# Kernel tuning notes

Measured on AMD Instinct MI355X. Metric: run time of the kernel, lower is better.

## Reference

```python
import jax, jax.numpy as jnp
import numpy as np

B, T, FC, FX = 64, 1024, 256, 512

def setup_inputs() -> dict:
    key = jax.random.key(0)
    kC, kX, kW, kb = jax.random.split(key, 4)
    C = jax.random.normal(kC, (B, T, FC), dtype=jnp.float32)
    X = jax.random.normal(kX, (B, T, FX), dtype=jnp.float32)
    # nn.Linear(encoding_size, context_size): W [fc, fx], b [fc]
    lim = 1.0 / np.sqrt(FX)
    W = jax.random.uniform(kW, (FC, FX), minval=-lim, maxval=lim, dtype=jnp.float32)
    b = jax.random.uniform(kb, (FC,), minval=-lim, maxval=lim, dtype=jnp.float32)
    return {"C": C, "X": X, "W": W, "b": b}

def reference(C, X, W, b):
    # Xt = Linear(X): [B, T, fc]
    Xt = jnp.einsum('btx,cx->btc', X, W) + b
    # Z[i, j, t] = <C[i, t, :], Xt[j, t, :]>  -> per-timestep BxB similarity
    Z = jnp.einsum('itc,jtc->ijt', C, Xt)
    # logsumexp over the negatives axis (dim 1), numerically stable
    lse = jax.nn.logsumexp(Z, axis=1)          # [B, T]
    Zdiag = jnp.einsum('iit->it', Z)           # [B, T], Z[i, i, t]
    return jnp.mean(Zdiag - lse)
```

## Files before the change

kernel.cpp:

```cpp
#include <hip/hip_runtime.h>

#define B_  64
#define T_  1024
#define FC_ 256
#define FX_ 512

typedef __bf16 bf16x8 __attribute__((ext_vector_type(8)));
typedef float  f32x4  __attribute__((ext_vector_type(4)));

__device__ __forceinline__ unsigned short f2bf(float f) {
  union { float f; unsigned int u; } v; v.f = f;
  unsigned int r = v.u + 0x7fffu + ((v.u >> 16) & 1u);
  return (unsigned short)(r >> 16);
}
__device__ __forceinline__ unsigned int pk2(float lo, float hi) {
  return (unsigned int)f2bf(lo) | ((unsigned int)f2bf(hi) << 16);
}

__global__ void k_wcvt(const float* __restrict__ W, unsigned short* __restrict__ Wb) {
  const int i = blockIdx.x * 256 + threadIdx.x;
  float4 v = ((const float4*)W)[i];
  ushort4 h;
  h.x = f2bf(v.x); h.y = f2bf(v.y); h.z = f2bf(v.z); h.w = f2bf(v.w);
  ((ushort4*)Wb)[i] = h;
}

__global__ __launch_bounds__(512, 2)
void k_fused(const float* __restrict__ C, const float* __restrict__ X,
             const unsigned short* __restrict__ Wb, const float* __restrict__ bias,
             float* __restrict__ out)
{
  __shared__ __align__(16) char sMem[81920];
  char* sX0 = sMem;
  char* sX1 = sMem + 8192;
  char* sW0 = sMem + 16384;
  char* sW1 = sMem + 49152;
  char* sC  = sMem;
  char* sXt = sMem + 32768;

  const int t    = blockIdx.x;
  const int tid  = threadIdx.x;
  const int lane = tid & 63;
  const int wid  = tid >> 6;

  const int xrow  = tid >> 3;
  const int xcol  = (tid & 7) * 8;
  const float* xbase = X + ((size_t)xrow * T_ + t) * FX_ + xcol;
  float4 x0a = *(const float4*)(xbase);
  float4 x0b = *(const float4*)(xbase + 4);

  const int wsw = (((lane & 7) ^ (lane >> 3)) << 4);
  {
    const char* wb0 = (const char*)Wb;
    #pragma unroll
    for (int l = 0; l < 4; ++l) {
      const int seg = wid * 4 + l;
      const int c   = seg * 8 + (lane >> 3);
      __builtin_amdgcn_global_load_lds(
          (const __attribute__((address_space(1))) unsigned int*)(wb0 + c * 1024 + wsw),
          (__attribute__((address_space(3))) unsigned int*)(sW0 + seg * 1024),
          16, 0, 0);
    }
  }

  const int crow = tid >> 3;
  const int ccol = (tid & 7) * 32;
  const float* cbase = C + ((size_t)crow * T_ + t) * FC_ + ccol;
  float4 creg[8];
  #pragma unroll
  for (int q = 0; q < 8; ++q) creg[q] = *(const float4*)(cbase + 4 * q);

  const float bv0 = bias[wid * 32 + (lane & 15)];
  const float bv1 = bias[wid * 32 + 16 + (lane & 15)];

  asm volatile("" ::: "memory");

  const int xwoff = xrow * 128 + (((tid & 7) * 16) ^ ((xrow & 7) << 4));
  {
    uint4 pk;
    pk.x = pk2(x0a.x, x0a.y); pk.y = pk2(x0a.z, x0a.w);
    pk.z = pk2(x0b.x, x0b.y); pk.w = pk2(x0b.z, x0b.w);
    *(uint4*)(sX0 + xwoff) = pk;
  }
  __syncthreads();

  f32x4 acc[4][2];
  #pragma unroll
  for (int i = 0; i < 4; ++i)
    #pragma unroll
    for (int n2 = 0; n2 < 2; ++n2)
      #pragma unroll
      for (int r = 0; r < 4; ++r) acc[i][n2][r] = 0.f;

  #pragma unroll 2
  for (int k = 0; k < 8; ++k) {
    char* scx = (k & 1) ? sX1 : sX0;
    char* snx = (k & 1) ? sX0 : sX1;
    char* scw = (k & 1) ? sW1 : sW0;
    char* snw = (k & 1) ? sW0 : sW1;

    float4 xn0, xn1;
    if (k < 7) {
      xn0 = *(const float4*)(xbase + (k + 1) * 64);
      xn1 = *(const float4*)(xbase + (k + 1) * 64 + 4);
      const char* wbk = (const char*)Wb + (k + 1) * 128;
      #pragma unroll
      for (int l = 0; l < 4; ++l) {
        const int seg = wid * 4 + l;
        const int c   = seg * 8 + (lane >> 3);
        __builtin_amdgcn_global_load_lds(
            (const __attribute__((address_space(1))) unsigned int*)(wbk + c * 1024 + wsw),
            (__attribute__((address_space(3))) unsigned int*)(snw + seg * 1024),
            16, 0, 0);
      }
    }
    asm volatile("" ::: "memory");

    #pragma unroll
    for (int kk = 0; kk < 2; ++kk) {
      const int kb = kk * 64 + ((lane >> 4) << 4);
      bf16x8 a[4], b2[2];
      #pragma unroll
      for (int i = 0; i < 4; ++i) {
        const int ar = i * 16 + (lane & 15);
        a[i] = *(const bf16x8*)(scx + ar * 128 + (kb ^ ((ar & 7) << 4)));
      }
      #pragma unroll
      for (int n2 = 0; n2 < 2; ++n2) {
        const int br = wid * 32 + n2 * 16 + (lane & 15);
        b2[n2] = *(const bf16x8*)(scw + br * 128 + (kb ^ ((br & 7) << 4)));
      }
      #pragma unroll
      for (int i = 0; i < 4; ++i)
        #pragma unroll
        for (int n2 = 0; n2 < 2; ++n2)
          acc[i][n2] = __builtin_amdgcn_mfma_f32_16x16x32_bf16(a[i], b2[n2], acc[i][n2], 0, 0, 0);
    }

    if (k < 7) {
      uint4 pk;
      pk.x = pk2(xn0.x, xn0.y); pk.y = pk2(xn0.z, xn0.w);
      pk.z = pk2(xn1.x, xn1.y); pk.w = pk2(xn1.z, xn1.w);
      *(uint4*)(snx + xwoff) = pk;
    }
    __syncthreads();
  }

  #pragma unroll
  for (int i = 0; i < 4; ++i)
    #pragma unroll
    for (int n2 = 0; n2 < 2; ++n2) {
      const int c  = wid * 32 + n2 * 16 + (lane & 15);
      const float bb = (n2 == 0) ? bv0 : bv1;
      #pragma unroll
      for (int r = 0; r < 4; ++r) {
        const int j   = i * 16 + ((lane >> 4) << 2) + r;
        const int off = j * 512 + ((2 * c) ^ ((j & 7) << 4));
        *(unsigned short*)(sXt + off) = f2bf(acc[i][n2][r] + bb);
      }
    }
  #pragma unroll
  for (int q = 0; q < 4; ++q) {
    const int cb  = (tid & 7) * 64 + q * 16;
    const int off = crow * 512 + (cb ^ ((crow & 7) << 4));
    float4 a0 = creg[2 * q], a1 = creg[2 * q + 1];
    uint4 pk;
    pk.x = pk2(a0.x, a0.y); pk.y = pk2(a0.z, a0.w);
    pk.z = pk2(a1.x, a1.y); pk.w = pk2(a1.z, a1.w);
    *(uint4*)(sC + off) = pk;
  }
  __syncthreads();

  if (wid < 4) {
    f32x4 z[4];
    #pragma unroll
    for (int n = 0; n < 4; ++n)
      #pragma unroll
      for (int r = 0; r < 4; ++r) z[n][r] = 0.f;

    #pragma unroll
    for (int kk = 0; kk < 8; ++kk) {
      const int kb = kk * 64 + ((lane >> 4) << 4);
      const int ar = wid * 16 + (lane & 15);
      bf16x8 a = *(const bf16x8*)(sC + ar * 512 + (kb ^ ((ar & 7) << 4)));
      #pragma unroll
      for (int n = 0; n < 4; ++n) {
        const int br = n * 16 + (lane & 15);
        bf16x8 b = *(const bf16x8*)(sXt + br * 512 + (kb ^ ((br & 7) << 4)));
        z[n] = __builtin_amdgcn_mfma_f32_16x16x32_bf16(a, b, z[n], 0, 0, 0);
      }
    }

    float partial = 0.f;
    #pragma unroll
    for (int r = 0; r < 4; ++r) {
      float m = fmaxf(fmaxf(z[0][r], z[1][r]), fmaxf(z[2][r], z[3][r]));
      #pragma unroll
      for (int d = 1; d < 16; d <<= 1) m = fmaxf(m, __shfl_xor(m, d));
      float s = __expf(z[0][r] - m) + __expf(z[1][r] - m) +
                __expf(z[2][r] - m) + __expf(z[3][r] - m);
      #pragma unroll
      for (int d = 1; d < 16; d <<= 1) s += __shfl_xor(s, d);
      const float lse = m + __logf(s);
      float dv = 0.f;
      #pragma unroll
      for (int n = 0; n < 4; ++n) dv = (n == wid) ? z[n][r] : dv;
      const int dl = ((lane >> 4) << 2) + r;
      if ((lane & 15) == dl) partial += dv - lse;
    }
    #pragma unroll
    for (int d = 1; d < 64; d <<= 1) partial += __shfl_xor(partial, d);
    if (lane == 0) atomicAdd(out, partial * (1.0f / (B_ * T_)));
  }
}

extern "C" void kernel_launch(void* const* d_in, const int* in_sizes, int n_in,
                              void* d_out, int out_size, void* d_ws, size_t ws_size,
                              hipStream_t stream) {
  const float* C  = (const float*)d_in[0];
  const float* X  = (const float*)d_in[1];
  const float* W  = (const float*)d_in[2];
  const float* bb = (const float*)d_in[3];
  unsigned short* Wb = (unsigned short*)d_ws;
  float* out = (float*)d_out;

  hipMemsetAsync(out, 0, sizeof(float), stream);
  k_wcvt <<<dim3(128),  dim3(256), 0, stream>>>(W, Wb);
  k_fused<<<dim3(1024), dim3(512), 0, stream>>>(C, X, Wb, bb, out);
}
```

Before: 271.5 us.

## Shrink fused block to 256 threads, read W fragments directly from global

The fused kernel moves from 512 threads to 256 threads per block and from 80KB to 40KB of LDS, targeting four blocks per CU instead of two. W fragments are now loaded straight from global/L2 into registers rather than staged through LDS with global_load_lds. X is single-buffered with register prefetch, and C is loaded into registers and fed directly as MFMA A operands instead of going through LDS. The memset launch is folded into the weight-conversion kernel. This raises occupancy and cuts LDS traffic, at the cost of uncoalesced per-lane global W reads and more syncs per k step.

```diff
diff --git a/kernel.cpp b/kernel.cpp
--- a/kernel.cpp
+++ b/kernel.cpp
@@ -16,202 +16,189 @@
 __device__ __forceinline__ unsigned int pk2(float lo, float hi) {
   return (unsigned int)f2bf(lo) | ((unsigned int)f2bf(hi) << 16);
 }
-
-__global__ void k_wcvt(const float* __restrict__ W, unsigned short* __restrict__ Wb) {
+__device__ __forceinline__ uint4 pk8(float4 a, float4 b) {
+  uint4 p;
+  p.x = pk2(a.x, a.y); p.y = pk2(a.z, a.w);
+  p.z = pk2(b.x, b.y); p.w = pk2(b.z, b.w);
+  return p;
+}
+
+__global__ void k_wcvt(const float* __restrict__ W, unsigned short* __restrict__ Wb,
+                       float* __restrict__ out) {
   const int i = blockIdx.x * 256 + threadIdx.x;
   float4 v = ((const float4*)W)[i];
   ushort4 h;
   h.x = f2bf(v.x); h.y = f2bf(v.y); h.z = f2bf(v.z); h.w = f2bf(v.w);
   ((ushort4*)Wb)[i] = h;
-}
-
-__global__ __launch_bounds__(512, 2)
+  if (i == 0) out[0] = 0.f;
+}
+
+__global__ __launch_bounds__(256, 4)
 void k_fused(const float* __restrict__ C, const float* __restrict__ X,
              const unsigned short* __restrict__ Wb, const float* __restrict__ bias,
              float* __restrict__ out)
 {
-  __shared__ __align__(16) char sMem[81920];
-  char* sX0 = sMem;
-  char* sX1 = sMem + 8192;
-  char* sW0 = sMem + 16384;
-  char* sW1 = sMem + 49152;
-  char* sC  = sMem;
-  char* sXt = sMem + 32768;
+  __shared__ __align__(16) char sMem[40960];
+  char* sX  = sMem;
+  char* sXt = sMem + 8192;
 
   const int t    = blockIdx.x;
   const int tid  = threadIdx.x;
   const int lane = tid & 63;
   const int wid  = tid >> 6;
-
-  const int xrow  = tid >> 3;
-  const int xcol  = (tid & 7) * 8;
-  const float* xbase = X + ((size_t)xrow * T_ + t) * FX_ + xcol;
-  float4 x0a = *(const float4*)(xbase);
-  float4 x0b = *(const float4*)(xbase + 4);
-
-  const int wsw = (((lane & 7) ^ (lane >> 3)) << 4);
+  const int l15  = lane & 15;
+  const int lhi  = lane >> 4;
+
+  const int xrow = tid >> 2;
+  const int xcb  = (tid & 3) * 32;
+  const float* xptr = X + ((size_t)xrow * T_ + t) * FX_ + ((tid & 3) << 4);
+  const int xwbase = xrow * 128;
+  const int xsw    = (xrow & 7) << 4;
+
+  const char* wbase = (const char*)Wb + (size_t)(wid * 64 + l15) * 1024 + lhi * 16;
+
+  float bv[4];
+  #pragma unroll
+  for (int n2 = 0; n2 < 4; ++n2) bv[n2] = bias[wid * 64 + n2 * 16 + l15];
+
+  float4 xb[4];
   {
-    const char* wb0 = (const char*)Wb;
-    #pragma unroll
-    for (int l = 0; l < 4; ++l) {
-      const int seg = wid * 4 + l;
-      const int c   = seg * 8 + (lane >> 3);
-      __builtin_amdgcn_global_load_lds(
-          (const __attribute__((address_space(1))) unsigned int*)(wb0 + c * 1024 + wsw),
-          (__attribute__((address_space(3))) unsigned int*)(sW0 + seg * 1024),
-          16, 0, 0);
-    }
-  }
-
-  const int crow = tid >> 3;
-  const int ccol = (tid & 7) * 32;
-  const float* cbase = C + ((size_t)crow * T_ + t) * FC_ + ccol;
-  float4 creg[8];
-  #pragma unroll
-  for (int q = 0; q < 8; ++q) creg[q] = *(const float4*)(cbase + 4 * q);
-
-  const float bv0 = bias[wid * 32 + (lane & 15)];
-  const float bv1 = bias[wid * 32 + 16 + (lane & 15)];
-
-  asm volatile("" ::: "memory");
-
-  const int xwoff = xrow * 128 + (((tid & 7) * 16) ^ ((xrow & 7) << 4));
-  {
-    uint4 pk;
-    pk.x = pk2(x0a.x, x0a.y); pk.y = pk2(x0a.z, x0a.w);
-    pk.z = pk2(x0b.x, x0b.y); pk.w = pk2(x0b.z, x0b.w);
-    *(uint4*)(sX0 + xwoff) = pk;
-  }
+    float4 xa[4];
+    #pragma unroll
+    for (int q = 0; q < 4; ++q) xa[q] = *(const float4*)(xptr + q * 4);
+    #pragma unroll
+    for (int q = 0; q < 4; ++q) xb[q] = *(const float4*)(xptr + 64 + q * 4);
+    uint4 p0 = pk8(xa[0], xa[1]);
+    uint4 p1 = pk8(xa[2], xa[3]);
+    *(uint4*)(sX + xwbase + ((xcb +  0) ^ xsw)) = p0;
+    *(uint4*)(sX + xwbase + ((xcb + 16) ^ xsw)) = p1;
+  }
+
+  f32x4 acc[4][4];
+  #pragma unroll
+  for (int i = 0; i < 4; ++i)
+    #pragma unroll
+    for (int n2 = 0; n2 < 4; ++n2)
+      #pragma unroll
+      for (int r = 0; r < 4; ++r) acc[i][n2][r] = 0.f;
+
   __syncthreads();
 
-  f32x4 acc[4][2];
+  #pragma unroll
+  for (int k = 0; k < 8; ++k) {
+    #pragma unroll
+    for (int kk = 0; kk < 2; ++kk) {
+      bf16x8 afr[4];
+      #pragma unroll
+      for (int i = 0; i < 4; ++i) {
+        const int ar = i * 16 + l15;
+        afr[i] = *(const bf16x8*)(sX + ar * 128 + ((kk * 64 + lhi * 16) ^ ((ar & 7) << 4)));
+      }
+      #pragma unroll
+      for (int n2 = 0; n2 < 4; ++n2) {
+        bf16x8 w = *(const bf16x8*)(wbase + n2 * 16384 + k * 128 + kk * 64);
+        #pragma unroll
+        for (int i = 0; i < 4; ++i)
+          acc[i][n2] = __builtin_amdgcn_mfma_f32_16x16x32_bf16(afr[i], w, acc[i][n2], 0, 0, 0);
+      }
+    }
+    __syncthreads();
+    if (k < 7) {
+      float4 xn[4];
+      if (k < 6) {
+        #pragma unroll
+        for (int q = 0; q < 4; ++q) xn[q] = *(const float4*)(xptr + (k + 2) * 64 + q * 4);
+      }
+      uint4 p0 = pk8(xb[0], xb[1]);
+      uint4 p1 = pk8(xb[2], xb[3]);
+      *(uint4*)(sX + xwbase + ((xcb +  0) ^ xsw)) = p0;
+      *(uint4*)(sX + xwbase + ((xcb + 16) ^ xsw)) = p1;
+      __syncthreads();
+      if (k < 6) {
+        #pragma unroll
+        for (int q = 0; q < 4; ++q) xb[q] = xn[q];
+      }
+    }
+  }
+
+  const float* cptr = C + ((size_t)(wid * 16 + l15) * T_ + t) * FC_ + lhi * 8;
+  float4 cv[8];
+  #pragma unroll
+  for (int q = 0; q < 4; ++q) {
+    cv[2 * q]     = *(const float4*)(cptr + q * 32);
+    cv[2 * q + 1] = *(const float4*)(cptr + q * 32 + 4);
+  }
+
   #pragma unroll
   for (int i = 0; i < 4; ++i)
     #pragma unroll
-    for (int n2 = 0; n2 < 2; ++n2)
-      #pragma unroll
-      for (int r = 0; r < 4; ++r) acc[i][n2][r] = 0.f;
-
-  #pragma unroll 2
-  for (int k = 0; k < 8; ++k) {
-    char* scx = (k & 1) ? sX1 : sX0;
-    char* snx = (k & 1) ? sX0 : sX1;
-    char* scw = (k & 1) ? sW1 : sW0;
-    char* snw = (k & 1) ? sW0 : sW1;
-
-    float4 xn0, xn1;
-    if (k < 7) {
-      xn0 = *(const float4*)(xbase + (k + 1) * 64);
-      xn1 = *(const float4*)(xbase + (k + 1) * 64 + 4);
-      const char* wbk = (const char*)Wb + (k + 1) * 128;
-      #pragma unroll
-      for (int l = 0; l < 4; ++l) {
-        const int seg = wid * 4 + l;
-        const int c   = seg * 8 + (lane >> 3);
-        __builtin_amdgcn_global_load_lds(
-            (const __attribute__((address_space(1))) unsigned int*)(wbk + c * 1024 + wsw),
-            (__attribute__((address_space(3))) unsigned int*)(snw + seg * 1024),
-            16, 0, 0);
-      }
-    }
-    asm volatile("" ::: "memory");
-
-    #pragma unroll
-    for (int kk = 0; kk < 2; ++kk) {
-      const int kb = kk * 64 + ((lane >> 4) << 4);
-      bf16x8 a[4], b2[2];
-      #pragma unroll
-      for (int i = 0; i < 4; ++i) {
-        const int ar = i * 16 + (lane & 15);
-        a[i] = *(const bf16x8*)(scx + ar * 128 + (kb ^ ((ar & 7) << 4)));
-      }
-      #pragma unroll
-      for (int n2 = 0; n2 < 2; ++n2) {
-        const int br = wid * 32 + n2 * 16 + (lane & 15);
-        b2[n2] = *(const bf16x8*)(scw + br * 128 + (kb ^ ((br & 7) << 4)));
-      }
-      #pragma unroll
-      for (int i = 0; i < 4; ++i)
-        #pragma unroll
-        for (int n2 = 0; n2 < 2; ++n2)
-          acc[i][n2] = __builtin_amdgcn_mfma_f32_16x16x32_bf16(a[i], b2[n2], acc[i][n2], 0, 0, 0);
-    }
-
-    if (k < 7) {
-      uint4 pk;
-      pk.x = pk2(xn0.x, xn0.y); pk.y = pk2(xn0.z, xn0.w);
-      pk.z = pk2(xn1.x, xn1.y); pk.w = pk2(xn1.z, xn1.w);
-      *(uint4*)(snx + xwoff) = pk;
-    }
-    __syncthreads();
-  }
-
-  #pragma unroll
-  for (int i = 0; i < 4; ++i)
-    #pragma unroll
-    for (int n2 = 0; n2 < 2; ++n2) {
-      const int c  = wid * 32 + n2 * 16 + (lane & 15);
-      const float bb = (n2 == 0) ? bv0 : bv1;
+    for (int n2 = 0; n2 < 4; ++n2) {
+      const int c2 = (wid * 64 + n2 * 16 + l15) * 2;
       #pragma unroll
       for (int r = 0; r < 4; ++r) {
-        const int j   = i * 16 + ((lane >> 4) << 2) + r;
-        const int off = j * 512 + ((2 * c) ^ ((j & 7) << 4));
-        *(unsigned short*)(sXt + off) = f2bf(acc[i][n2][r] + bb);
-      }
-    }
-  #pragma unroll
-  for (int q = 0; q < 4; ++q) {
-    const int cb  = (tid & 7) * 64 + q * 16;
-    const int off = crow * 512 + (cb ^ ((crow & 7) << 4));
-    float4 a0 = creg[2 * q], a1 = creg[2 * q + 1];
-    uint4 pk;
-    pk.x = pk2(a0.x, a0.y); pk.y = pk2(a0.z, a0.w);
-    pk.z = pk2(a1.x, a1.y); pk.w = pk2(a1.z, a1.w);
-    *(uint4*)(sC + off) = pk;
+        const int j = i * 16 + lhi * 4 + r;
+        *(unsigned short*)(sXt + j * 512 + (c2 ^ ((j & 7) << 4))) =
+            f2bf(acc[i][n2][r] + bv[n2]);
+      }
+    }
+
+  bf16x8 ca[4];
+  #pragma unroll
+  for (int q = 0; q < 4; ++q) ca[q] = __builtin_bit_cast(bf16x8, pk8(cv[2 * q], cv[2 * q + 1]));
+  float4 cw[8];
+  #pragma unroll
+  for (int q = 0; q < 4; ++q) {
+    cw[2 * q]     = *(const float4*)(cptr + 128 + q * 32);
+    cw[2 * q + 1] = *(const float4*)(cptr + 128 + q * 32 + 4);
   }
   __syncthreads();
 
-  if (wid < 4) {
-    f32x4 z[4];
-    #pragma unroll
-    for (int n = 0; n < 4; ++n)
-      #pragma unroll
-      for (int r = 0; r < 4; ++r) z[n][r] = 0.f;
-
-    #pragma unroll
-    for (int kk = 0; kk < 8; ++kk) {
-      const int kb = kk * 64 + ((lane >> 4) << 4);
-      const int ar = wid * 16 + (lane & 15);
-      bf16x8 a = *(const bf16x8*)(sC + ar * 512 + (kb ^ ((ar & 7) << 4)));
-      #pragma unroll
-      for (int n = 0; n < 4; ++n) {
-        const int br = n * 16 + (lane & 15);
-        bf16x8 b = *(const bf16x8*)(sXt + br * 512 + (kb ^ ((br & 7) << 4)));
-        z[n] = __builtin_amdgcn_mfma_f32_16x16x32_bf16(a, b, z[n], 0, 0, 0);
-      }
-    }
-
-    float partial = 0.f;
-    #pragma unroll
-    for (int r = 0; r < 4; ++r) {
-      float m = fmaxf(fmaxf(z[0][r], z[1][r]), fmaxf(z[2][r], z[3][r]));
-      #pragma unroll
-      for (int d = 1; d < 16; d <<= 1) m = fmaxf(m, __shfl_xor(m, d));
-      float s = __expf(z[0][r] - m) + __expf(z[1][r] - m) +
-                __expf(z[2][r] - m) + __expf(z[3][r] - m);
-      #pragma unroll
-      for (int d = 1; d < 16; d <<= 1) s += __shfl_xor(s, d);
-      const float lse = m + __logf(s);
-      float dv = 0.f;
-      #pragma unroll
-      for (int n = 0; n < 4; ++n) dv = (n == wid) ? z[n][r] : dv;
-      const int dl = ((lane >> 4) << 2) + r;
-      if ((lane & 15) == dl) partial += dv - lse;
-    }
-    #pragma unroll
-    for (int d = 1; d < 64; d <<= 1) partial += __shfl_xor(partial, d);
-    if (lane == 0) atomicAdd(out, partial * (1.0f / (B_ * T_)));
-  }
+  f32x4 z[4];
+  #pragma unroll
+  for (int n = 0; n < 4; ++n)
+    #pragma unroll
+    for (int r = 0; r < 4; ++r) z[n][r] = 0.f;
+
+  #pragma unroll
+  for (int q = 0; q < 4; ++q) {
+    #pragma unroll
+    for (int n = 0; n < 4; ++n) {
+      const int br = n * 16 + l15;
+      bf16x8 b = *(const bf16x8*)(sXt + br * 512 + ((q * 64 + lhi * 16) ^ ((br & 7) << 4)));
+      z[n] = __builtin_amdgcn_mfma_f32_16x16x32_bf16(ca[q], b, z[n], 0, 0, 0);
+    }
+  }
+  #pragma unroll
+  for (int q = 0; q < 4; ++q) ca[q] = __builtin_bit_cast(bf16x8, pk8(cw[2 * q], cw[2 * q + 1]));
+  #pragma unroll
+  for (int q = 0; q < 4; ++q) {
+    #pragma unroll
+    for (int n = 0; n < 4; ++n) {
+      const int br = n * 16 + l15;
+      bf16x8 b = *(const bf16x8*)(sXt + br * 512 + (((q + 4) * 64 + lhi * 16) ^ ((br & 7) << 4)));
+      z[n] = __builtin_amdgcn_mfma_f32_16x16x32_bf16(ca[q], b, z[n], 0, 0, 0);
+    }
+  }
+
+  float partial = 0.f;
+  #pragma unroll
+  for (int r = 0; r < 4; ++r) {
+    float m = fmaxf(fmaxf(z[0][r], z[1][r]), fmaxf(z[2][r], z[3][r]));
+    #pragma unroll
+    for (int d = 1; d < 16; d <<= 1) m = fmaxf(m, __shfl_xor(m, d));
+    float s = __expf(z[0][r] - m) + __expf(z[1][r] - m) +
+              __expf(z[2][r] - m) + __expf(z[3][r] - m);
+    #pragma unroll
+    for (int d = 1; d < 16; d <<= 1) s += __shfl_xor(s, d);
+    const float lse = m + __logf(s);
+    float dv = 0.f;
+    #pragma unroll
+    for (int n = 0; n < 4; ++n) dv = (n == wid) ? z[n][r] : dv;
+    if (l15 == lhi * 4 + r) partial += dv - lse;
+  }
+  #pragma unroll
+  for (int d = 1; d < 64; d <<= 1) partial += __shfl_xor(partial, d);
+  if (lane == 0) atomicAdd(out, partial * (1.0f / (B_ * T_)));
 }
 
 extern "C" void kernel_launch(void* const* d_in, const int* in_sizes, int n_in,
@@ -224,7 +211,6 @@
   unsigned short* Wb = (unsigned short*)d_ws;
   float* out = (float*)d_out;
 
-  hipMemsetAsync(out, 0, sizeof(float), stream);
-  k_wcvt <<<dim3(128),  dim3(256), 0, stream>>>(W, Wb);
-  k_fused<<<dim3(1024), dim3(512), 0, stream>>>(C, X, Wb, bb, out);
-}
+  k_wcvt <<<dim3(128),  dim3(256), 0, stream>>>(W, Wb, out);
+  k_fused<<<dim3(1024), dim3(256), 0, stream>>>(C, X, Wb, bb, out);
+}
```

Result: slower. 297.5 us (+9.6%).
